# Optimization experiments

Measured on AMD Instinct MI355X. Metric: run time of the kernel, lower is better.

The kernel has to match this reference:

```python
import jax, jax.numpy as jnp
import numpy as np

B, T, IMG, PATCH = 4, 16, 256, 16
G = IMG // PATCH            # 16
P = G * G                   # 256 patches
PP = PATCH * PATCH          # 256 pixels per patch
H, FF, L, NH = 512, 2048, 4, 8
MASK_BIAS = 20.0
SKIP_PAIRS = [(0, 2), (0, 3), (1, 3), (0, 4), (1, 4), (2, 4)]


def _ln(x, g, b):
    m = x.mean(-1, keepdims=True)
    v = ((x - m) ** 2).mean(-1, keepdims=True)
    return (x - m) * jax.lax.rsqrt(v + 1e-5) * g + b


def _attn(x, wq, bq, wk, bk, wv, bv, wo, wo_mask, mask):
    # x: (B, G, S, D) -- attention over axis S within each (B, G) group
    Bx, Gx, S, D = x.shape
    hd = D // NH
    scale = hd ** -0.5

    def proj(w, b_):
        y = jnp.einsum('bgsd,ed->bgse', x, w) + b_
        return y.reshape(Bx, Gx, S, NH, hd).transpose(0, 1, 3, 2, 4)  # (B,G,NH,S,hd)

    q, k, v = proj(wq, bq), proj(wk, bk), proj(wv, bv)
    scores = jnp.einsum('bgnsh,bgnth->bgnst', q, k) * scale + (mask - 0.5) * MASK_BIAS
    a = jax.nn.softmax(scores, axis=-1)
    o = jnp.einsum('bgnst,bgnth->bgnsh', a, v).transpose(0, 1, 3, 2, 4).reshape(Bx, Gx, S, D)
    return jnp.einsum('bgsd,ed->bgse', o, wo * wo_mask)  # masked W_o, no bias


def _forward(x, s_mask, t_mask, wo_masks, ff_masks, skip_masks, head_mask,
             patch_w, patch_b, temporal_pos, spatial_pos,
             sq_w, sq_b, sk_w, sk_b, sv_w, sv_b, so_w,
             tq_w, tq_b, tk_w, tk_b, tv_w, tv_b, to_w,
             ln_s_g, ln_s_b, ln_t_g, ln_t_b, ln_f_g, ln_f_b,
             ff1_w, ff1_b, ff2_w, ff2_b, skip_w, lnf_g, lnf_b, head_w, head_b):
    Bx = x.shape[0]
    # patch embed: (B,T,IMG,IMG) -> (B,T,P,PP) -> (B,T,P,H)
    xp = x.reshape(Bx, T, G, PATCH, G, PATCH).transpose(0, 1, 2, 4, 3, 5).reshape(Bx, T, P, PP)
    tokens = jnp.einsum('btpq,hq->btph', xp, patch_w) + patch_b
    tokens = tokens + temporal_pos + spatial_pos

    acts = [tokens]
    for i in range(L):
        h = acts[i]
        wm = wo_masks[i]
        # spatial attention over P within each frame
        s_out = _attn(_ln(h, ln_s_g[i], ln_s_b[i]),
                      sq_w[i], sq_b[i], sk_w[i], sk_b[i], sv_w[i], sv_b[i],
                      so_w[i], wm, s_mask)
        h = h + s_out
        # temporal attention over T at each patch position
        ht = _ln(h, ln_t_g[i], ln_t_b[i]).transpose(0, 2, 1, 3)  # (B,P,T,H)
        t_out = _attn(ht, tq_w[i], tq_b[i], tk_w[i], tk_b[i], tv_w[i], tv_b[i],
                      to_w[i], wm, t_mask).transpose(0, 2, 1, 3)
        h = h + t_out
        # masked FFN
        hf = _ln(h, ln_f_g[i], ln_f_b[i])
        f1 = jax.nn.relu(jnp.einsum('btpd,fd->btpf', hf, ff1_w[i] * ff_masks[i]) + ff1_b[i])
        h = h + jnp.einsum('btpf,df->btpd', f1, ff2_w[i]) + ff2_b[i]
        # cross-layer masked skip connections into layer i+1
        for si, (src, tgt) in enumerate(SKIP_PAIRS):
            if tgt != i + 1:
                continue
            h = h + jnp.einsum('btpd,ed->btpe', acts[src], skip_w[si] * skip_masks[si])
        acts.append(h)

    final = _ln(acts[-1], lnf_g, lnf_b)
    last = final[:, -1]  # (B,P,H) last frame
    patches = jax.nn.sigmoid(jnp.einsum('bpd,qd->bpq', last, head_w * head_mask) + head_b)
    pred = patches.reshape(Bx, G, G, PATCH, PATCH).transpose(0, 1, 3, 2, 4).reshape(Bx, IMG, IMG)
    return pred


def setup_inputs() -> dict:
    key = jax.random.key(0)
    ks = iter(jax.random.split(key, 64))
    nrm = lambda sh: jax.random.normal(next(ks), sh, dtype=jnp.float32) * 0.02
    uni = lambda sh: jax.random.uniform(next(ks), sh, dtype=jnp.float32)
    d = {}
    d['x'] = jax.random.normal(next(ks), (B, T, IMG, IMG), dtype=jnp.float32)
    d['s_mask'] = uni((P, P))
    d['t_mask'] = uni((T, T))
    d['wo_masks'] = uni((L, H, H))
    d['ff_masks'] = uni((L, FF, H))
    d['skip_masks'] = uni((len(SKIP_PAIRS), H, H))
    d['head_mask'] = uni((PP, H))
    d['patch_w'] = nrm((H, PP)); d['patch_b'] = jnp.zeros((H,), jnp.float32)
    d['temporal_pos'] = nrm((1, T, 1, H))
    d['spatial_pos'] = nrm((1, 1, P, H))
    for pre in ['sq', 'sk', 'sv', 'tq', 'tk', 'tv']:
        d[pre + '_w'] = nrm((L, H, H)); d[pre + '_b'] = jnp.zeros((L, H), jnp.float32)
    d['so_w'] = nrm((L, H, H)); d['to_w'] = nrm((L, H, H))
    for pre in ['ln_s', 'ln_t', 'ln_f']:
        d[pre + '_g'] = jnp.ones((L, H), jnp.float32); d[pre + '_b'] = jnp.zeros((L, H), jnp.float32)
    d['ff1_w'] = nrm((L, FF, H)); d['ff1_b'] = jnp.zeros((L, FF), jnp.float32)
    d['ff2_w'] = nrm((L, H, FF)); d['ff2_b'] = jnp.zeros((L, H), jnp.float32)
    d['skip_w'] = nrm((len(SKIP_PAIRS), H, H))
    d['lnf_g'] = jnp.ones((H,), jnp.float32); d['lnf_b'] = jnp.zeros((H,), jnp.float32)
    d['head_w'] = nrm((PP, H)); d['head_b'] = jnp.zeros((PP,), jnp.float32)
    return d


def reference(x, s_mask, t_mask, wo_masks, ff_masks, skip_masks, head_mask,
              patch_w, patch_b, temporal_pos, spatial_pos,
              sq_w, sq_b, sk_w, sk_b, sv_w, sv_b, so_w,
              tq_w, tq_b, tk_w, tk_b, tv_w, tv_b, to_w,
              ln_s_g, ln_s_b, ln_t_g, ln_t_b, ln_f_g, ln_f_b,
              ff1_w, ff1_b, ff2_w, ff2_b, skip_w, lnf_g, lnf_b, head_w, head_b):
    return _forward(x, s_mask, t_mask, wo_masks, ff_masks, skip_masks, head_mask,
                    patch_w, patch_b, temporal_pos, spatial_pos,
                    sq_w, sq_b, sk_w, sk_b, sv_w, sv_b, so_w,
                    tq_w, tq_b, tk_w, tk_b, tv_w, tv_b, to_w,
                    ln_s_g, ln_s_b, ln_t_g, ln_t_b, ln_f_g, ln_f_b,
                    ff1_w, ff1_b, ff2_w, ff2_b, skip_w, lnf_g, lnf_b, head_w, head_b)
```

## Files before the change

kernel.cpp:

```cpp
#include <hip/hip_runtime.h>
#include <hip/hip_bf16.h>
#include <math.h>

#define BB 4
#define TT 16
#define IMGSZ 256
#define PPATCH 256
#define PQ 256
#define HH 512
#define FFDIM 2048
#define LLAYERS 4
#define NHEADS 8
#define HD 64

#define NTOK (BB*TT*PPATCH)

typedef unsigned short bfu;
typedef unsigned int u32;
typedef short bf16x8 __attribute__((ext_vector_type(8)));
typedef float f32x4 __attribute__((ext_vector_type(4)));

__device__ inline float bf2f(bfu u) {
    union { unsigned int i; float f; } cv; cv.i = ((unsigned int)u) << 16; return cv.f;
}
__device__ inline bfu f2bf(float f) {
    __hip_bfloat16 h = __float2bfloat16(f);
    union { __hip_bfloat16 h; bfu u; } cv; cv.h = h; return cv.u;
}
__device__ inline float u_lo(unsigned int u) {
    union { unsigned int i; float f; } cv; cv.i = u << 16; return cv.f;
}
__device__ inline float u_hi(unsigned int u) {
    union { unsigned int i; float f; } cv; cv.i = u & 0xffff0000u; return cv.f;
}
__device__ inline unsigned int pack2(float a, float b) {
    return (unsigned int)f2bf(a) | ((unsigned int)f2bf(b) << 16);
}
__device__ inline unsigned int addbf2(unsigned int a, unsigned int b) {
    return pack2(u_lo(a) + u_lo(b), u_hi(a) + u_hi(b));
}
__device__ __forceinline__ void gload16(const void* g, void* l) {
    __builtin_amdgcn_global_load_lds(
        (const __attribute__((address_space(1))) u32*)g,
        (__attribute__((address_space(3))) u32*)l, 16, 0, 0);
}

#define WL_SQKV 0
#define WL_SO   786432
#define WL_TQKV 1048576
#define WL_TO   1835008
#define WL_FF1  2097152
#define WL_FF2  3145728
#define WL_TOT  4194304
#define WP_SKIP 0
#define WP_HEAD 1572864
#define WP_PATCH 1703936
#define WP_TOT  1835008

__global__ __launch_bounds__(256) void patchify_k(const float* __restrict__ x,
                                                  bfu* __restrict__ xp) {
    int idx = blockIdx.x * 256 + threadIdx.x;
    int col = idx & 255;
    int row = idx >> 8;
    int p   = row & 255;
    int bt  = row >> 8;
    int gr = p >> 4, gc = p & 15;
    int pr = col >> 4, pc = col & 15;
    xp[idx] = f2bf(x[(size_t)bt * 65536 + (gr * 16 + pr) * 256 + gc * 16 + pc]);
}

__global__ __launch_bounds__(256) void addpos_k(bfu* __restrict__ tok,
                                                const float* __restrict__ tpos,
                                                const float* __restrict__ spos) {
    int idx = blockIdx.x * 256 + threadIdx.x;
    int h = idx & 511;
    int p = (idx >> 9) & 255;
    int t = (idx >> 17) & 15;
    tok[idx] = f2bf(bf2f(tok[idx]) + tpos[t * HH + h] + spos[p * HH + h]);
}

__global__ __launch_bounds__(256) void convpers_k(const float* __restrict__ skw,
                                                  const float* __restrict__ skm,
                                                  const float* __restrict__ hw,
                                                  const float* __restrict__ hm,
                                                  const float* __restrict__ pw,
                                                  bfu* __restrict__ out) {
    int g8 = blockIdx.x * 256 + threadIdx.x;
    int idx = g8 * 8;
    const float* src; const float* msk = nullptr; int off;
    if (idx < WP_HEAD)       { src = skw; msk = skm; off = idx; }
    else if (idx < WP_PATCH) { src = hw;  msk = hm;  off = idx - WP_HEAD; }
    else                     { src = pw;             off = idx - WP_PATCH; }
    float4 a = *(const float4*)(src + off);
    float4 b = *(const float4*)(src + off + 4);
    if (msk) {
        float4 ma = *(const float4*)(msk + off), mb = *(const float4*)(msk + off + 4);
        a.x *= ma.x; a.y *= ma.y; a.z *= ma.z; a.w *= ma.w;
        b.x *= mb.x; b.y *= mb.y; b.z *= mb.z; b.w *= mb.w;
    }
    uint4 o = { pack2(a.x, a.y), pack2(a.z, a.w), pack2(b.x, b.y), pack2(b.z, b.w) };
    *(uint4*)(out + idx) = o;
}

__global__ __launch_bounds__(256) void convw_k(const float* __restrict__ sq, const float* __restrict__ sk,
                                               const float* __restrict__ sv, const float* __restrict__ so,
                                               const float* __restrict__ tq, const float* __restrict__ tk,
                                               const float* __restrict__ tv, const float* __restrict__ to,
                                               const float* __restrict__ ff1, const float* __restrict__ ff2,
                                               const float* __restrict__ wom, const float* __restrict__ ffm,
                                               const float* __restrict__ sqb, const float* __restrict__ skb,
                                               const float* __restrict__ svb, const float* __restrict__ tqb,
                                               const float* __restrict__ tkb, const float* __restrict__ tvb,
                                               bfu* __restrict__ out,
                                               float* __restrict__ bias_s, float* __restrict__ bias_t) {
    int g8 = blockIdx.x * 256 + threadIdx.x;
    if (g8 < 384) {
        int bi = g8 * 8;
        const float* bsrc; float* bdst;
        if (bi < 1536) {
            int o = bi; bdst = bias_s + o;
            bsrc = (o < 512 ? sqb : o < 1024 ? skb : svb) + (o & 511);
        } else {
            int o = bi - 1536; bdst = bias_t + o;
            bsrc = (o < 512 ? tqb : o < 1024 ? tkb : tvb) + (o & 511);
        }
        *(float4*)bdst = *(const float4*)bsrc;
        *(float4*)(bdst + 4) = *(const float4*)(bsrc + 4);
    }
    int idx = g8 * 8;
    const float* src; const float* msk = nullptr; int off;
    if (idx < WL_SO) {
        int r = idx; src = (r < 262144 ? sq : r < 524288 ? sk : sv); off = r & 262143;
    } else if (idx < WL_TQKV) { src = so; msk = wom; off = idx - WL_SO; }
    else if (idx < WL_TO) {
        int r = idx - WL_TQKV; src = (r < 262144 ? tq : r < 524288 ? tk : tv); off = r & 262143;
    } else if (idx < WL_FF1) { src = to; msk = wom; off = idx - WL_TO; }
    else if (idx < WL_FF2)   { src = ff1; msk = ffm; off = idx - WL_FF1; }
    else                     { src = ff2; off = idx - WL_FF2; }
    float4 a = *(const float4*)(src + off);
    float4 b = *(const float4*)(src + off + 4);
    if (msk) {
        float4 ma = *(const float4*)(msk + off), mb = *(const float4*)(msk + off + 4);
        a.x *= ma.x; a.y *= ma.y; a.z *= ma.z; a.w *= ma.w;
        b.x *= mb.x; b.y *= mb.y; b.z *= mb.z; b.w *= mb.w;
    }
    uint4 o = { pack2(a.x, a.y), pack2(a.z, a.w), pack2(b.x, b.y), pack2(b.z, b.w) };
    *(uint4*)(out + idx) = o;
}

__global__ __launch_bounds__(256) void ln_k(const bfu* __restrict__ X,
                                            const float* __restrict__ g,
                                            const float* __restrict__ b,
                                            bfu* __restrict__ Y,
                                            int rows, int mode) {
    int wave = threadIdx.x >> 6;
    int lane = threadIdx.x & 63;
    int row = blockIdx.x * 4 + wave;
    if (row >= rows) return;
    int inRow = row, outRow = row;
    if (mode == 2) {
        int bb = row >> 8; int p = row & 255;
        inRow = ((bb * TT + (TT - 1)) << 8) + p;
    } else if (mode == 1) {
        int bb = row >> 12;
        int r  = row & 4095;
        int t  = r >> 8;
        int p  = r & 255;
        outRow = (((bb << 8) + p) << 4) + t;
    }
    const bfu* xr = X + (size_t)inRow * HH;
    bfu vv[8];
    *(uint4*)vv = *(const uint4*)(xr + lane * 8);
    float v[8];
    float s = 0.f;
    #pragma unroll
    for (int i = 0; i < 8; i++) { v[i] = bf2f(vv[i]); s += v[i]; }
    #pragma unroll
    for (int off = 32; off; off >>= 1) s += __shfl_xor(s, off, 64);
    float mean = s * (1.f / 512.f);
    float vs = 0.f;
    #pragma unroll
    for (int i = 0; i < 8; i++) { float d = v[i] - mean; vs += d * d; }
    #pragma unroll
    for (int off = 32; off; off >>= 1) vs += __shfl_xor(vs, off, 64);
    float rstd = rsqrtf(vs * (1.f / 512.f) + 1e-5f);
    bfu out[8];
    #pragma unroll
    for (int i = 0; i < 8; i++) {
        int c = lane * 8 + i;
        out[i] = f2bf((v[i] - mean) * rstd * g[c] + b[c]);
    }
    *(uint4*)(Y + (size_t)outRow * HH + lane * 8) = *(uint4*)out;
}

#define XCD_SWZ(wid)                                                           \
    const int nwg = gridDim.x;                                                 \
    const int id = blockIdx.x;                                                 \
    const int q = nwg >> 3, r = nwg & 7;                                       \
    const int xcd = id & 7, sub = id >> 3;                                     \
    const int wid = (xcd < r ? xcd * (q + 1) : r * (q + 1) + (xcd - r) * q) + sub;

#define VWAIT4 do { asm volatile("s_waitcnt vmcnt(4)" ::: "memory");           \
                    __builtin_amdgcn_sched_barrier(0); } while (0)
#define VWAIT0 do { asm volatile("s_waitcnt vmcnt(0)" ::: "memory");           \
                    __builtin_amdgcn_sched_barrier(0); } while (0)
#define BAR    do { __builtin_amdgcn_s_barrier();                              \
                    __builtin_amdgcn_sched_barrier(0); } while (0)

__device__ __forceinline__ void seg_ptrs(int s,
    const bfu* A0, const bfu* W0, int K0, const bfu* A1, const bfu* W1, int K1,
    const bfu* A2, const bfu* W2, int K2, const bfu* A3, const bfu* W3, int K3,
    const bfu*& pa, const bfu*& pw, int& kk) {
    switch (s) {
        case 0:  pa = A0; pw = W0; kk = K0; break;
        case 1:  pa = A1; pw = W1; kk = K1; break;
        case 2:  pa = A2; pw = W2; kk = K2; break;
        default: pa = A3; pw = W3; kk = K3; break;
    }
}

#define CTS 136

template<int ACT>
__global__ __launch_bounds__(256) void gemm3_k(
    const bfu* __restrict__ A0, const bfu* __restrict__ W0, int K0,
    const bfu* __restrict__ A1, const bfu* __restrict__ W1, int K1,
    const bfu* __restrict__ A2, const bfu* __restrict__ W2, int K2,
    const bfu* __restrict__ A3, const bfu* __restrict__ W3, int K3,
    int nseg,
    const float* __restrict__ bias, const bfu* __restrict__ addTo,
    bfu* __restrict__ C, int M, int N, int nx) {
    __shared__ __align__(16) bfu S[3][2][128 * 32];
    XCD_SWZ(wid);
    const int bm = (wid / nx) * 128, bn = (wid % nx) * 128;

    const int tid = threadIdx.x, wave = tid >> 6, lane = tid & 63;
    const int wr = (wave >> 1) * 64, wc = (wave & 1) * 64;
    const int srow = wave * 32 + (lane >> 2);
    const int skoff = (((lane & 3) ^ ((lane >> 3) & 3)) * 8);
    const int frow = lane & 15;
    const int fk = (((lane >> 4) ^ ((frow >> 1) & 3)) * 8);

    const bfu *pa, *pw; int kseg;
    int seg = 0;
    seg_ptrs(0, A0, W0, K0, A1, W1, K1, A2, W2, K2, A3, W3, K3, pa, pw, kseg);
    const bfu* as0 = pa + (size_t)(bm + srow) * kseg + skoff;
    const bfu* as1 = as0 + (size_t)16 * kseg;
    const bfu* ws0 = pw + (size_t)(bn + srow) * kseg + skoff;
    const bfu* ws1 = ws0 + (size_t)16 * kseg;
    int kleft = kseg;
    const int tot = (K0 + K1 + K2 + K3) >> 5;

    f32x4 acc[4][4];
    const f32x4 zero = {0.f, 0.f, 0.f, 0.f};
    #pragma unroll
    for (int m = 0; m < 4; m++)
        #pragma unroll
        for (int n = 0; n < 4; n++) acc[m][n] = zero;

    #define STAGE(buf)                                                         \
        do {                                                                   \
            gload16(as0, &S[buf][0][(wave * 32) * 32]);                        \
            gload16(as1, &S[buf][0][(wave * 32 + 16) * 32]);                   \
            gload16(ws0, &S[buf][1][(wave * 32) * 32]);                        \
            gload16(ws1, &S[buf][1][(wave * 32 + 16) * 32]);                   \
            as0 += 32; as1 += 32; ws0 += 32; ws1 += 32;                        \
            kleft -= 32;                                                       \
            if (kleft == 0 && seg + 1 < nseg) {                                \
                seg++;                                                         \
                seg_ptrs(seg, A0, W0, K0, A1, W1, K1, A2, W2, K2, A3, W3, K3,  \
                         pa, pw, kseg);                                        \
                as0 = pa + (size_t)(bm + srow) * kseg + skoff;                 \
                as1 = as0 + (size_t)16 * kseg;                                 \
                ws0 = pw + (size_t)(bn + srow) * kseg + skoff;                 \
                ws1 = ws0 + (size_t)16 * kseg;                                 \
                kleft = kseg;                                                  \
            }                                                                  \
        } while (0)

    #define COMPUTE(buf)                                                       \
        do {                                                                   \
            bf16x8 af[4], bfr[4];                                              \
            _Pragma("unroll")                                                  \
            for (int m = 0; m < 4; m++)                                        \
                af[m] = *(const bf16x8*)&S[buf][0][(wr + m * 16 + frow) * 32 + fk]; \
            _Pragma("unroll")                                                  \
            for (int n = 0; n < 4; n++)                                        \
                bfr[n] = *(const bf16x8*)&S[buf][1][(wc + n * 16 + frow) * 32 + fk]; \
            __builtin_amdgcn_s_setprio(1);                                     \
            _Pragma("unroll")                                                  \
            for (int m = 0; m < 4; m++)                                        \
                _Pragma("unroll")                                              \
                for (int n = 0; n < 4; n++)                                    \
                    acc[m][n] = __builtin_amdgcn_mfma_f32_16x16x32_bf16(       \
                        af[m], bfr[n], acc[m][n], 0, 0, 0);                    \
            __builtin_amdgcn_s_setprio(0);                                     \
        } while (0)

    STAGE(0);
    STAGE(1);
    VWAIT4;
    BAR;
    int cur = 0, sb = 2;
    for (int t = 0; t < tot; t++) {
        const bool pf = (t + 2 < tot);
        if (pf) { STAGE(sb); sb = (sb == 2) ? 0 : sb + 1; }
        COMPUTE(cur);
        cur = (cur == 2) ? 0 : cur + 1;
        if (t + 1 < tot) {
            if (pf) { VWAIT4; } else { VWAIT0; }
            BAR;
        }
    }
    #undef STAGE
    #undef COMPUTE

    bfu* Ct = &S[0][0][0];
    __syncthreads();
    const int erow = (lane >> 4) * 4, ecol = lane & 15;
    float bv[4];
    #pragma unroll
    for (int n = 0; n < 4; n++) bv[n] = bias ? bias[bn + wc + n * 16 + ecol] : 0.f;
    #pragma unroll
    for (int m = 0; m < 4; m++) {
        #pragma unroll
        for (int n = 0; n < 4; n++) {
            #pragma unroll
            for (int r2 = 0; r2 < 4; r2++) {
                float v = acc[m][n][r2] + bv[n];
                if (ACT == 1) v = v > 0.f ? v : 0.f;
                if (ACT == 2) v = 1.f / (1.f + __expf(-v));
                Ct[(wr + m * 16 + erow + r2) * CTS + wc + n * 16 + ecol] = f2bf(v);
            }
        }
    }
    __syncthreads();
    #pragma unroll
    for (int it = 0; it < 8; it++) {
        int row = it * 16 + (tid >> 4);
        int col = (tid & 15) * 8;
        uint4 v = *(const uint4*)&Ct[row * CTS + col];
        size_t goff = (size_t)(bm + row) * N + bn + col;
        if (addTo) {
            uint4 t4 = *(const uint4*)(addTo + goff);
            v.x = addbf2(v.x, t4.x); v.y = addbf2(v.y, t4.y);
            v.z = addbf2(v.z, t4.z); v.w = addbf2(v.w, t4.w);
        }
        *(uint4*)(C + goff) = v;
    }
}

#define VTS 264
#define PTS 72
__global__ __launch_bounds__(256, 2) void sattn_k(const bfu* __restrict__ QKV,
                                                  const float* __restrict__ mask,
                                                  bfu* __restrict__ O) {
    __shared__ __align__(16) bfu Vt[64][VTS];
    __shared__ __align__(16) bfu Pt[4][64][PTS];
    const int gh = blockIdx.x, g = gh >> 3, head = gh & 7;
    const int tid = threadIdx.x, wave = tid >> 6, lane = tid & 63;
    const size_t rbase = (size_t)g * 256;
    const size_t qoff = (size_t)head * 64, koff = qoff + 512, voff = qoff + 1024;

    {
        const bfu* vp = QKV + (rbase + tid) * 1536 + voff;
        bfu vals[64];
        #pragma unroll
        for (int c = 0; c < 8; c++) *(uint4*)&vals[c * 8] = *(const uint4*)(vp + c * 8);
        #pragma unroll
        for (int d = 0; d < 64; d++) Vt[d][tid] = vals[d];
    }
    __syncthreads();

    const int l15 = lane & 15, l4 = lane >> 4;
    const int wq0 = wave * 64;

    bf16x8 Qb[4][2];
    #pragma unroll
    for (int n = 0; n < 4; n++)
        #pragma unroll
        for (int kr = 0; kr < 2; kr++)
            Qb[n][kr] = *(const bf16x8*)(QKV + (rbase + wq0 + n * 16 + l15) * 1536 + qoff + kr * 32 + l4 * 8);

    f32x4 acc_o[4][4];
    const f32x4 zero = {0.f, 0.f, 0.f, 0.f};
    #pragma unroll
    for (int m = 0; m < 4; m++)
        #pragma unroll
        for (int n = 0; n < 4; n++) acc_o[m][n] = zero;
    float m_run[4] = {-3e38f, -3e38f, -3e38f, -3e38f};
    float l_run[4] = {0.f, 0.f, 0.f, 0.f};

    for (int kt = 0; kt < 4; kt++) {
        f32x4 acc_s[4][4];
        #pragma unroll
        for (int m = 0; m < 4; m++)
            #pragma unroll
            for (int n = 0; n < 4; n++) acc_s[m][n] = zero;
        #pragma unroll
        for (int m = 0; m < 4; m++) {
            const bfu* kp = QKV + (rbase + kt * 64 + m * 16 + l15) * 1536 + koff + l4 * 8;
            bf16x8 Ka0 = *(const bf16x8*)kp;
            bf16x8 Ka1 = *(const bf16x8*)(kp + 32);
            #pragma unroll
            for (int n = 0; n < 4; n++) {
                acc_s[m][n] = __builtin_amdgcn_mfma_f32_16x16x32_bf16(Ka0, Qb[n][0], acc_s[m][n], 0, 0, 0);
                acc_s[m][n] = __builtin_amdgcn_mfma_f32_16x16x32_bf16(Ka1, Qb[n][1], acc_s[m][n], 0, 0, 0);
            }
        }
        #pragma unroll
        for (int m = 0; m < 4; m++)
            #pragma unroll
            for (int n = 0; n < 4; n++) {
                float4 mv = *(const float4*)(mask + (size_t)(wq0 + n * 16 + l15) * 256 + kt * 64 + m * 16 + l4 * 4);
                acc_s[m][n][0] = acc_s[m][n][0] * 0.125f + (mv.x - 0.5f) * 20.f;
                acc_s[m][n][1] = acc_s[m][n][1] * 0.125f + (mv.y - 0.5f) * 20.f;
                acc_s[m][n][2] = acc_s[m][n][2] * 0.125f + (mv.z - 0.5f) * 20.f;
                acc_s[m][n][3] = acc_s[m][n][3] * 0.125f + (mv.w - 0.5f) * 20.f;
            }
        #pragma unroll
        for (int n = 0; n < 4; n++) {
            float tmax = acc_s[0][n][0];
            #pragma unroll
            for (int m = 0; m < 4; m++)
                #pragma unroll
                for (int r = 0; r < 4; r++) tmax = fmaxf(tmax, acc_s[m][n][r]);
            tmax = fmaxf(tmax, __shfl_xor(tmax, 16, 64));
            tmax = fmaxf(tmax, __shfl_xor(tmax, 32, 64));
            float newm = fmaxf(m_run[n], tmax);
            float corr = __expf(m_run[n] - newm);
            m_run[n] = newm;
            float esum = 0.f;
            #pragma unroll
            for (int m = 0; m < 4; m++) {
                #pragma unroll
                for (int r = 0; r < 4; r++) {
                    float p = __expf(acc_s[m][n][r] - newm);
                    acc_s[m][n][r] = p;
                    esum += p;
                }
            }
            esum += __shfl_xor(esum, 16, 64);
            esum += __shfl_xor(esum, 32, 64);
            l_run[n] = l_run[n] * corr + esum;
            #pragma unroll
            for (int m = 0; m < 4; m++) {
                acc_o[m][n][0] *= corr; acc_o[m][n][1] *= corr;
                acc_o[m][n][2] *= corr; acc_o[m][n][3] *= corr;
            }
            #pragma unroll
            for (int m = 0; m < 4; m++) {
                uint2 pw = { pack2(acc_s[m][n][0], acc_s[m][n][1]),
                             pack2(acc_s[m][n][2], acc_s[m][n][3]) };
                *(uint2*)&Pt[wave][n * 16 + l15][m * 16 + l4 * 4] = pw;
            }
        }
        #pragma unroll
        for (int kr = 0; kr < 2; kr++) {
            bf16x8 Va[4], Pb[4];
            #pragma unroll
            for (int m = 0; m < 4; m++)
                Va[m] = *(const bf16x8*)&Vt[m * 16 + l15][kt * 64 + kr * 32 + l4 * 8];
            #pragma unroll
            for (int n = 0; n < 4; n++)
                Pb[n] = *(const bf16x8*)&Pt[wave][n * 16 + l15][kr * 32 + l4 * 8];
            #pragma unroll
            for (int m = 0; m < 4; m++)
                #pragma unroll
                for (int n = 0; n < 4; n++)
                    acc_o[m][n] = __builtin_amdgcn_mfma_f32_16x16x32_bf16(Va[m], Pb[n], acc_o[m][n], 0, 0, 0);
        }
    }

    float inv[4];
    #pragma unroll
    for (int n = 0; n < 4; n++) inv[n] = 1.f / l_run[n];
    #pragma unroll
    for (int m = 0; m < 4; m++)
        #pragma unroll
        for (int n = 0; n < 4; n++) {
            ushort4 ov = { f2bf(acc_o[m][n][0] * inv[n]), f2bf(acc_o[m][n][1] * inv[n]),
                           f2bf(acc_o[m][n][2] * inv[n]), f2bf(acc_o[m][n][3] * inv[n]) };
            *(ushort4*)(O + (rbase + wq0 + n * 16 + l15) * 512 + head * 64 + m * 16 + l4 * 4) = ov;
        }
}

__global__ __launch_bounds__(256) void tattn_k(const bfu* __restrict__ QKV,
                                               const float* __restrict__ mask,
                                               bfu* __restrict__ O) {
    __shared__ __align__(16) bfu Ks[16][520];
    __shared__ __align__(16) bfu Vs[16][520];
    __shared__ __align__(16) bfu Qs[16][520];
    const int bp = blockIdx.x, b = bp >> 8, p = bp & 255;
    const int tid = threadIdx.x, wave = tid >> 6, lane = tid & 63;
    const size_t rb = (size_t)bp * 16;
    {
        int r = tid >> 4, off = (tid & 15) * 32;
        const bfu* qp = QKV + (rb + r) * 1536 + off;
        const bfu* kp = qp + 512;
        const bfu* vp = qp + 1024;
        #pragma unroll
        for (int c = 0; c < 32; c += 8) {
            *(uint4*)&Qs[r][off + c] = *(const uint4*)(qp + c);
            *(uint4*)&Ks[r][off + c] = *(const uint4*)(kp + c);
            *(uint4*)&Vs[r][off + c] = *(const uint4*)(vp + c);
        }
    }
    __syncthreads();
    const int qq = lane >> 4, kk = lane & 15;
    const int dp4 = (lane & 15) * 4;
    const int abase = lane & 48;
    for (int hh = 0; hh < 2; hh++) {
        const int head = wave * 2 + hh, hoff = head * 64;
        for (int qp4 = 0; qp4 < 4; qp4++) {
            const int q = qp4 * 4 + qq;
            float dot = 0.f;
            #pragma unroll
            for (int dg = 0; dg < 8; dg++) {
                const unsigned int* kp = (const unsigned int*)&Ks[kk][hoff + dg * 8];
                const unsigned int* qp = (const unsigned int*)&Qs[q][hoff + dg * 8];
                #pragma unroll
                for (int c = 0; c < 4; c++) {
                    unsigned int ku = kp[c], qu = qp[c];
                    dot += u_lo(ku) * u_lo(qu) + u_hi(ku) * u_hi(qu);
                }
            }
            float sc = dot * 0.125f + (mask[q * 16 + kk] - 0.5f) * 20.f;
            float m = sc;
            #pragma unroll
            for (int off = 1; off < 16; off <<= 1) m = fmaxf(m, __shfl_xor(m, off, 64));
            float e = __expf(sc - m);
            float sum = e;
            #pragma unroll
            for (int off = 1; off < 16; off <<= 1) sum += __shfl_xor(sum, off, 64);
            float a = e / sum;
            float o0 = 0.f, o1 = 0.f, o2 = 0.f, o3 = 0.f;
            #pragma unroll
            for (int k = 0; k < 16; k++) {
                float ak = __shfl(a, abase + k, 64);
                const unsigned int* vp = (const unsigned int*)&Vs[k][hoff + dp4];
                unsigned int u0 = vp[0], u1 = vp[1];
                o0 += ak * u_lo(u0); o1 += ak * u_hi(u0);
                o2 += ak * u_lo(u1); o3 += ak * u_hi(u1);
            }
            size_t orow = ((size_t)((b * 16 + q) * 256 + p)) * 512 + hoff + dp4;
            ushort4 ov = { f2bf(o0), f2bf(o1), f2bf(o2), f2bf(o3) };
            *(ushort4*)(O + orow) = ov;
        }
    }
}

__global__ __launch_bounds__(256) void unpatch_k(const bfu* __restrict__ patches,
                                                 float* __restrict__ pred) {
    int idx = blockIdx.x * 256 + threadIdx.x;
    int c = idx & 255;
    int r = (idx >> 8) & 255;
    int bb = idx >> 16;
    int gr = r >> 4, pr = r & 15, gc = c >> 4, pc = c & 15;
    pred[idx] = bf2f(patches[((size_t)(bb * 256 + gr * 16 + gc) << 8) + pr * 16 + pc]);
}

static inline void run_gseg(int act,
                            const bfu* A0, const bfu* W0, int K0,
                            const bfu* A1, const bfu* W1, int K1,
                            const bfu* A2, const bfu* W2, int K2,
                            const bfu* A3, const bfu* W3, int K3, int nseg,
                            const float* bias, const bfu* addTo, bfu* C,
                            int M, int N, hipStream_t s) {
    int nx = N / 128;
    int nwg = nx * (M / 128);
    if (act == 0)
        gemm3_k<0><<<nwg, 256, 0, s>>>(A0, W0, K0, A1, W1, K1, A2, W2, K2, A3, W3, K3,
                                       nseg, bias, addTo, C, M, N, nx);
    else if (act == 1)
        gemm3_k<1><<<nwg, 256, 0, s>>>(A0, W0, K0, A1, W1, K1, A2, W2, K2, A3, W3, K3,
                                       nseg, bias, addTo, C, M, N, nx);
    else
        gemm3_k<2><<<nwg, 256, 0, s>>>(A0, W0, K0, A1, W1, K1, A2, W2, K2, A3, W3, K3,
                                       nseg, bias, addTo, C, M, N, nx);
}

static inline void run_g(int act, const bfu* A, const bfu* W, int K,
                         const float* bias, const bfu* addTo, bfu* C,
                         int M, int N, hipStream_t s) {
    run_gseg(act, A, W, K, nullptr, nullptr, 0, nullptr, nullptr, 0,
             nullptr, nullptr, 0, 1, bias, addTo, C, M, N, s);
}

extern "C" void kernel_launch(void* const* d_in, const int* in_sizes, int n_in,
                              void* d_out, int out_size, void* d_ws, size_t ws_size,
                              hipStream_t stream) {
    const float* x        = (const float*)d_in[0];
    const float* s_mask   = (const float*)d_in[1];
    const float* t_mask   = (const float*)d_in[2];
    const float* wo_masks = (const float*)d_in[3];
    const float* ff_masks = (const float*)d_in[4];
    const float* skip_masks = (const float*)d_in[5];
    const float* head_mask  = (const float*)d_in[6];
    const float* patch_w  = (const float*)d_in[7];
    const float* patch_b  = (const float*)d_in[8];
    const float* tpos     = (const float*)d_in[9];
    const float* spos     = (const float*)d_in[10];
    const float* sq_w = (const float*)d_in[11];
    const float* sq_b = (const float*)d_in[12];
    const float* sk_w = (const float*)d_in[13];
    const float* sk_b = (const float*)d_in[14];
    const float* sv_w = (const float*)d_in[15];
    const float* sv_b = (const float*)d_in[16];
    const float* tq_w = (const float*)d_in[17];
    const float* tq_b = (const float*)d_in[18];
    const float* tk_w = (const float*)d_in[19];
    const float* tk_b = (const float*)d_in[20];
    const float* tv_w = (const float*)d_in[21];
    const float* tv_b = (const float*)d_in[22];
    const float* so_w = (const float*)d_in[23];
    const float* to_w = (const float*)d_in[24];
    const float* ln_s_g = (const float*)d_in[25];
    const float* ln_s_b = (const float*)d_in[26];
    const float* ln_t_g = (const float*)d_in[27];
    const float* ln_t_b = (const float*)d_in[28];
    const float* ln_f_g = (const float*)d_in[29];
    const float* ln_f_b = (const float*)d_in[30];
    const float* ff1_w = (const float*)d_in[31];
    const float* ff1_b = (const float*)d_in[32];
    const float* ff2_w = (const float*)d_in[33];
    const float* ff2_b = (const float*)d_in[34];
    const float* skip_w = (const float*)d_in[35];
    const float* lnf_g = (const float*)d_in[36];
    const float* lnf_b = (const float*)d_in[37];
    const float* head_w = (const float*)d_in[38];
    const float* head_b = (const float*)d_in[39];

    bfu* ws = (bfu*)d_ws;
    const size_t ACTE = (size_t)NTOK * HH;
    bfu* acts[5];
    for (int i = 0; i < 5; i++) acts[i] = ws + i * ACTE;
    bfu* xln = ws + 5 * ACTE;
    bfu* qkv = ws + 6 * ACTE;
    bfu* ob  = ws + 9 * ACTE;
    bfu* f1  = qkv;
    bfu* xp      = ob;
    bfu* lastln  = xln;
    bfu* patches = qkv;
    bfu* wlayer = ws + 10 * ACTE;
    bfu* wpers  = wlayer + WL_TOT;
    float* bias_s = (float*)(wpers + WP_TOT);
    float* bias_t = bias_s + 1536;

    convpers_k<<<WP_TOT / 8 / 256, 256, 0, stream>>>(skip_w, skip_masks, head_w, head_mask,
                                                     patch_w, wpers);

    patchify_k<<<NTOK * PQ / 256, 256, 0, stream>>>(x, xp);
    run_g(0, xp, wpers + WP_PATCH, PQ, patch_b, nullptr, acts[0], NTOK, HH, stream);
    addpos_k<<<NTOK * HH / 256, 256, 0, stream>>>(acts[0], tpos, spos);

    const size_t WS = 512 * 512;
    const size_t FS = 2048 * 512;
    const int srcs[6] = {0, 0, 1, 0, 1, 2};
    const int tgts[6] = {2, 3, 3, 4, 4, 4};

    for (int i = 0; i < LLAYERS; i++) {
        bfu* h   = acts[i];
        bfu* hn  = acts[i + 1];
        convw_k<<<WL_TOT / 8 / 256, 256, 0, stream>>>(
            sq_w + i * WS, sk_w + i * WS, sv_w + i * WS, so_w + i * WS,
            tq_w + i * WS, tk_w + i * WS, tv_w + i * WS, to_w + i * WS,
            ff1_w + i * FS, ff2_w + i * FS,
            wo_masks + i * WS, ff_masks + i * FS,
            sq_b + i * HH, sk_b + i * HH, sv_b + i * HH,
            tq_b + i * HH, tk_b + i * HH, tv_b + i * HH,
            wlayer, bias_s, bias_t);
        ln_k<<<NTOK / 4, 256, 0, stream>>>(h, ln_s_g + i * HH, ln_s_b + i * HH, xln, NTOK, 0);
        run_g(0, xln, wlayer + WL_SQKV, HH, bias_s, nullptr, qkv, NTOK, 1536, stream);
        sattn_k<<<BB * TT * NHEADS, 256, 0, stream>>>(qkv, s_mask, ob);
        run_g(0, ob, wlayer + WL_SO, HH, nullptr, h, hn, NTOK, HH, stream);
        ln_k<<<NTOK / 4, 256, 0, stream>>>(hn, ln_t_g + i * HH, ln_t_b + i * HH, xln, NTOK, 1);
        run_g(0, xln, wlayer + WL_TQKV, HH, bias_t, nullptr, qkv, NTOK, 1536, stream);
        tattn_k<<<BB * PPATCH, 256, 0, stream>>>(qkv, t_mask, ob);
        run_g(0, ob, wlayer + WL_TO, HH, nullptr, hn, hn, NTOK, HH, stream);
        ln_k<<<NTOK / 4, 256, 0, stream>>>(hn, ln_f_g + i * HH, ln_f_b + i * HH, xln, NTOK, 0);
        run_g(1, xln, wlayer + WL_FF1, HH, ff1_b + i * FFDIM, nullptr, f1, NTOK, FFDIM, stream);
        {
            const bfu* Aseg[4] = { f1, nullptr, nullptr, nullptr };
            const bfu* Wseg[4] = { wlayer + WL_FF2, nullptr, nullptr, nullptr };
            int Kseg[4] = { FFDIM, 0, 0, 0 };
            int ns = 1;
            for (int si = 0; si < 6; si++) {
                if (tgts[si] != i + 1) continue;
                Aseg[ns] = acts[srcs[si]];
                Wseg[ns] = wpers + WP_SKIP + si * WS;
                Kseg[ns] = HH;
                ns++;
            }
            run_gseg(0, Aseg[0], Wseg[0], Kseg[0], Aseg[1], Wseg[1], Kseg[1],
                     Aseg[2], Wseg[2], Kseg[2], Aseg[3], Wseg[3], Kseg[3], ns,
                     ff2_b + i * HH, hn, hn, NTOK, HH, stream);
        }
    }

    ln_k<<<(BB * PPATCH) / 4, 256, 0, stream>>>(acts[4], lnf_g, lnf_b, lastln, BB * PPATCH, 2);
    run_g(2, lastln, wpers + WP_HEAD, HH, head_b, nullptr, patches, BB * PPATCH, PQ, stream);
    unpatch_k<<<BB * IMGSZ * IMGSZ / 256, 256, 0, stream>>>(patches, (float*)d_out);
}
```

Measured before the change: 1.289 ms.

## Add 256x128-tile triple-buffered GEMM for QKV and FF1 projections

Adds a new GEMM kernel with 256x128 output tiles per workgroup (8x4 MFMA accumulators per wave) and a three-stage LDS ring with async global loads, waiting on vmcnt(6) to keep two stages in flight. It replaces the generic segmented GEMM for the spatial/temporal QKV projections and the FF1 layer. The larger tile is meant to raise arithmetic intensity and cut A/W reloads, and the deeper pipeline is meant to hide load latency. In exchange it uses more registers and LDS per workgroup (about 72KB), which lowers occupancy, and it launches half as many workgroups.

```diff
diff --git a/kernel.cpp b/kernel.cpp
--- a/kernel.cpp
+++ b/kernel.cpp
@@ -202,6 +202,8 @@
 
 #define VWAIT4 do { asm volatile("s_waitcnt vmcnt(4)" ::: "memory");           \
                     __builtin_amdgcn_sched_barrier(0); } while (0)
+#define VWAIT6 do { asm volatile("s_waitcnt vmcnt(6)" ::: "memory");           \
+                    __builtin_amdgcn_sched_barrier(0); } while (0)
 #define VWAIT0 do { asm volatile("s_waitcnt vmcnt(0)" ::: "memory");           \
                     __builtin_amdgcn_sched_barrier(0); } while (0)
 #define BAR    do { __builtin_amdgcn_s_barrier();                              \
@@ -350,6 +352,112 @@
     }
 }
 
+template<int ACT>
+__global__ __launch_bounds__(256) void gemm5_k(
+    const bfu* __restrict__ A, const bfu* __restrict__ W,
+    const float* __restrict__ bias, bfu* __restrict__ C,
+    int M, int N, int K, int nx) {
+    __shared__ __align__(16) bfu S[3][384 * 32];
+    XCD_SWZ(wid);
+    const int bm = (wid / nx) * 256, bn = (wid % nx) * 128;
+
+    const int tid = threadIdx.x, wave = tid >> 6, lane = tid & 63;
+    const int wr = (wave >> 1) * 128, wc = (wave & 1) * 64;
+    const int r16 = lane >> 2;
+    const int skoff = (((lane & 3) ^ ((lane >> 3) & 3)) * 8);
+    const int frow = lane & 15;
+    const int fk = (((lane >> 4) ^ ((frow >> 1) & 3)) * 8);
+
+    const bfu* aSrc = A + (size_t)(bm + wave * 64 + r16) * K + skoff;
+    const bfu* wSrc = W + (size_t)(bn + wave * 32 + r16) * K + skoff;
+    const size_t k16 = (size_t)16 * K;
+    const int tot = K >> 5;
+
+    f32x4 acc[8][4];
+    const f32x4 zero = {0.f, 0.f, 0.f, 0.f};
+    #pragma unroll
+    for (int m = 0; m < 8; m++)
+        #pragma unroll
+        for (int n = 0; n < 4; n++) acc[m][n] = zero;
+
+    #define STAGE5(buf)                                                        \
+        do {                                                                   \
+            bfu* sa  = &S[buf][(wave * 64) * 32];                              \
+            bfu* sbw = &S[buf][256 * 32 + (wave * 32) * 32];                   \
+            gload16(aSrc,            sa);                                      \
+            gload16(aSrc + k16,      sa + 16 * 32);                            \
+            gload16(aSrc + 2 * k16,  sa + 32 * 32);                            \
+            gload16(aSrc + 3 * k16,  sa + 48 * 32);                            \
+            gload16(wSrc,            sbw);                                     \
+            gload16(wSrc + k16,      sbw + 16 * 32);                           \
+            aSrc += 32; wSrc += 32;                                            \
+        } while (0)
+
+    #define COMPUTE5(buf)                                                      \
+        do {                                                                   \
+            bf16x8 af[8], bfr[4];                                              \
+            _Pragma("unroll")                                                  \
+            for (int m = 0; m < 8; m++)                                        \
+                af[m] = *(const bf16x8*)&S[buf][(wr + m * 16 + frow) * 32 + fk]; \
+            _Pragma("unroll")                                                  \
+            for (int n = 0; n < 4; n++)                                        \
+                bfr[n] = *(const bf16x8*)&S[buf][256 * 32 + (wc + n * 16 + frow) * 32 + fk]; \
+            __builtin_amdgcn_s_setprio(1);                                     \
+            _Pragma("unroll")                                                  \
+            for (int m = 0; m < 8; m++)                                        \
+                _Pragma("unroll")                                              \
+                for (int n = 0; n < 4; n++)                                    \
+                    acc[m][n] = __builtin_amdgcn_mfma_f32_16x16x32_bf16(       \
+                        af[m], bfr[n], acc[m][n], 0, 0, 0);                    \
+            __builtin_amdgcn_s_setprio(0);                                     \
+        } while (0)
+
+    STAGE5(0);
+    STAGE5(1);
+    VWAIT6;
+    BAR;
+    int cur = 0, sb = 2;
+    for (int t = 0; t < tot; t++) {
+        const bool pf = (t + 2 < tot);
+        if (pf) { STAGE5(sb); sb = (sb == 2) ? 0 : sb + 1; }
+        COMPUTE5(cur);
+        cur = (cur == 2) ? 0 : cur + 1;
+        if (t + 1 < tot) {
+            if (pf) { VWAIT6; } else { VWAIT0; }
+            BAR;
+        }
+    }
+    #undef STAGE5
+    #undef COMPUTE5
+
+    bfu* Ct = &S[0][0];
+    __syncthreads();
+    const int erow = (lane >> 4) * 4, ecol = lane & 15;
+    float bv[4];
+    #pragma unroll
+    for (int n = 0; n < 4; n++) bv[n] = bias ? bias[bn + wc + n * 16 + ecol] : 0.f;
+    #pragma unroll
+    for (int m = 0; m < 8; m++) {
+        #pragma unroll
+        for (int n = 0; n < 4; n++) {
+            #pragma unroll
+            for (int r2 = 0; r2 < 4; r2++) {
+                float v = acc[m][n][r2] + bv[n];
+                if (ACT == 1) v = v > 0.f ? v : 0.f;
+                Ct[(wr + m * 16 + erow + r2) * CTS + wc + n * 16 + ecol] = f2bf(v);
+            }
+        }
+    }
+    __syncthreads();
+    #pragma unroll
+    for (int it = 0; it < 16; it++) {
+        int row = it * 16 + (tid >> 4);
+        int col = (tid & 15) * 8;
+        uint4 v = *(const uint4*)&Ct[row * CTS + col];
+        *(uint4*)(C + (size_t)(bm + row) * N + bn + col) = v;
+    }
+}
+
 #define VTS 264
 #define PTS 72
 __global__ __launch_bounds__(256, 2) void sattn_k(const bfu* __restrict__ QKV,
@@ -585,6 +693,14 @@
                          int M, int N, hipStream_t s) {
     run_gseg(act, A, W, K, nullptr, nullptr, 0, nullptr, nullptr, 0,
              nullptr, nullptr, 0, 1, bias, addTo, C, M, N, s);
+}
+
+static inline void run_g5(int act, const bfu* A, const bfu* W, int K,
+                          const float* bias, bfu* C, int M, int N, hipStream_t s) {
+    int nx = N / 128;
+    int nwg = nx * (M / 256);
+    if (act == 0)      gemm5_k<0><<<nwg, 256, 0, s>>>(A, W, bias, C, M, N, K, nx);
+    else if (act == 1) gemm5_k<1><<<nwg, 256, 0, s>>>(A, W, bias, C, M, N, K, nx);
 }
 
 extern "C" void kernel_launch(void* const* d_in, const int* in_sizes, int n_in,
@@ -671,15 +787,15 @@
             tq_b + i * HH, tk_b + i * HH, tv_b + i * HH,
             wlayer, bias_s, bias_t);
         ln_k<<<NTOK / 4, 256, 0, stream>>>(h, ln_s_g + i * HH, ln_s_b + i * HH, xln, NTOK, 0);
-        run_g(0, xln, wlayer + WL_SQKV, HH, bias_s, nullptr, qkv, NTOK, 1536, stream);
+        run_g5(0, xln, wlayer + WL_SQKV, HH, bias_s, qkv, NTOK, 1536, stream);
         sattn_k<<<BB * TT * NHEADS, 256, 0, stream>>>(qkv, s_mask, ob);
         run_g(0, ob, wlayer + WL_SO, HH, nullptr, h, hn, NTOK, HH, stream);
         ln_k<<<NTOK / 4, 256, 0, stream>>>(hn, ln_t_g + i * HH, ln_t_b + i * HH, xln, NTOK, 1);
-        run_g(0, xln, wlayer + WL_TQKV, HH, bias_t, nullptr, qkv, NTOK, 1536, stream);
+        run_g5(0, xln, wlayer + WL_TQKV, HH, bias_t, qkv, NTOK, 1536, stream);
         tattn_k<<<BB * PPATCH, 256, 0, stream>>>(qkv, t_mask, ob);
         run_g(0, ob, wlayer + WL_TO, HH, nullptr, hn, hn, NTOK, HH, stream);
         ln_k<<<NTOK / 4, 256, 0, stream>>>(hn, ln_f_g + i * HH, ln_f_b + i * HH, xln, NTOK, 0);
-        run_g(1, xln, wlayer + WL_FF1, HH, ff1_b + i * FFDIM, nullptr, f1, NTOK, FFDIM, stream);
+        run_g5(1, xln, wlayer + WL_FF1, HH, ff1_b + i * FFDIM, f1, NTOK, FFDIM, stream);
         {
             const bfu* Aseg[4] = { f1, nullptr, nullptr, nullptr };
             const bfu* Wseg[4] = { wlayer + WL_FF2, nullptr, nullptr, nullptr };
```

Result: slower. 1.419 ms (+10.1%).
